# Optimization experiments

Measured on AMD Instinct MI355X. Metric: run time of the kernel, lower is better.

The kernel has to match this reference:

```python
import jax, jax.numpy as jnp
import numpy as np

E, DM, DH, K, DIL = 8, 512, 1024, 3, 2
N, L = 128, 128
PAD = DIL * (K - 1) // 2  # 'same' padding


def _conv1d(x, w):
    # x: [N, Cin, L], w: [Cout, Cin, K] -> [N, Cout, L]
    return jax.lax.conv_general_dilated(
        x, w, window_strides=(1,), padding=[(PAD, PAD)],
        rhs_dilation=(DIL,), dimension_numbers=("NCH", "OIH", "NCH"))


def _moe_conv(x, W, B, onehot):
    # W: [E, Cout, Cin, K], B: [E, Cout], onehot: [N, E]
    ys = jax.vmap(lambda w, b: _conv1d(x, w) + b[None, :, None])(W, B)  # [E, N, Cout, L]
    return jnp.einsum("enol,ne->nol", ys, onehot)


def setup_inputs() -> dict:
    key = jax.random.key(0)
    k1, k2, k3, k4, k5 = jax.random.split(key, 5)
    inp = jax.random.normal(k1, (N, DM, L), dtype=jnp.float32)
    # uneven per-expert sample counts summing to N (samples pre-sorted by expert)
    fwd_expert_count = jnp.asarray(np.array([10, 20, 16, 16, 12, 22, 14, 18], dtype=np.int32))
    w1 = jax.random.normal(k2, (E, DH, DM, K), dtype=jnp.float32) * 0.02
    b1 = jax.random.normal(k3, (E, DH), dtype=jnp.float32) * 0.02
    w2 = jax.random.normal(k4, (E, DM, DH, K), dtype=jnp.float32) * 0.02
    b2 = jax.random.normal(k5, (E, DM), dtype=jnp.float32) * 0.02
    return {"inp": inp, "fwd_expert_count": fwd_expert_count,
            "w1": w1, "b1": b1, "w2": w2, "b2": b2}


def reference(inp, fwd_expert_count, w1, b1, w2, b2):
    # map each sample index to its expert via cumulative counts
    cs = jnp.cumsum(fwd_expert_count)
    eid = jnp.searchsorted(cs, jnp.arange(N), side="right")  # [N]
    onehot = (eid[:, None] == jnp.arange(E)[None, :]).astype(inp.dtype)  # [N, E]
    h = _moe_conv(inp, w1, b1, onehot)       # [N, DH, L]
    h = jax.nn.gelu(h)
    out = _moe_conv(h, w2, b2, onehot)       # [N, DM, L]
    return out
```

## Files before the change

### kernel.cpp

```cpp
#include <hip/hip_runtime.h>
#include <hip/hip_bf16.h>
#include <stdint.h>


typedef __attribute__((ext_vector_type(8))) short short8;
typedef __attribute__((ext_vector_type(4))) float f32x4;

#define DMV 512
#define DHV 1024

#define OFF_X   0ull
#define OFF_H   (16ull << 20)
#define OFF_W1  (48ull << 20)
#define OFF_W2  (72ull << 20)

#define VMW(n) asm volatile("s_waitcnt vmcnt(" #n ")" ::: "memory")
#define VMNOP  do {} while (0)

__device__ __forceinline__ uint16_t f2bf(float f) {
  uint32_t u = __builtin_bit_cast(uint32_t, f);
  uint32_t r = (u + 0x7FFFu + ((u >> 16) & 1u)) >> 16;
  return (uint16_t)r;
}

__device__ __forceinline__ void async_copy16(const void* g, void* l) {
  __builtin_amdgcn_global_load_lds(
      (const __attribute__((address_space(1))) uint32_t*)g,
      (__attribute__((address_space(3))) uint32_t*)l, 16, 0, 0);
}

__device__ __forceinline__ float gelu_f(float x) {
  float u = 0.7978845608028654f * (x + 0.044715f * x * x * x);
  float t = __expf(2.0f * u);
  float th = 1.0f - 2.0f / (t + 1.0f);
  return 0.5f * x * (1.0f + th);
}

__global__ __launch_bounds__(256) void prep_x_t(const float* __restrict__ inp,
                                                uint16_t* __restrict__ xp) {
  uint32_t b = blockIdx.x;
  uint32_t s = b >> 4, cc = b & 15u;
  __shared__ uint16_t xs[32][132];
  uint32_t t = threadIdx.x;
  const float* src0 = inp + ((size_t)s * DMV + cc * 32u) * 128u;
#pragma unroll
  for (int i = 0; i < 4; ++i) {
    uint32_t idx = (uint32_t)i * 256u + t;
    uint32_t ch = idx >> 5, l4 = idx & 31u;
    float4 f = *(const float4*)(src0 + ch * 128u + l4 * 4u);
    uint2 pk;
    pk.x = (uint32_t)f2bf(f.x) | ((uint32_t)f2bf(f.y) << 16);
    pk.y = (uint32_t)f2bf(f.z) | ((uint32_t)f2bf(f.w) << 16);
    *(uint2*)&xs[ch][l4 * 4u] = pk;
  }
  __syncthreads();
  uint32_t l = t >> 1, half = t & 1u;
  uint32_t fl = ((l + 2u) >> 1) & 3u;
#pragma unroll
  for (int hi = 0; hi < 2; ++hi) {
    uint32_t sub = half * 2u + (uint32_t)hi;
    uint32_t cg = (sub ^ fl) & 3u;
    uint32_t pk[4];
#pragma unroll
    for (int p2 = 0; p2 < 4; ++p2) {
      uint32_t c0 = cg * 8u + (uint32_t)p2 * 2u;
      pk[p2] = (uint32_t)xs[c0][l] | ((uint32_t)xs[c0 + 1][l] << 16);
    }
    uint4 v; v.x = pk[0]; v.y = pk[1]; v.z = pk[2]; v.w = pk[3];
    size_t slot = (((size_t)s * 16u + cc) * 128u + l) * 4u + sub;
    *(uint4*)(xp + slot * 8u) = v;
  }
}

template <int LOGCG, int LOGO>
__global__ __launch_bounds__(256) void prep_w_c(const float* __restrict__ w,
                                                uint16_t* __restrict__ wp) {
  constexpr uint32_t C = 4u << LOGCG;
  constexpr uint32_t CCn = C >> 5;
  constexpr uint32_t MTn = 1u << (LOGO - 7);
  uint32_t t = blockIdx.x * 256u + threadIdx.x;
  uint32_t cg = t & ((1u << LOGCG) - 1u);
  uint32_t o = (t >> LOGCG) & ((1u << LOGO) - 1u);
  uint32_t e = t >> (LOGCG + LOGO);
  uint32_t row = o & 127u, mt = o >> 7;
  const float* src = w + (((size_t)(e << LOGO) + o) * C + cg * 4u) * 3u;
  float4 f0 = *(const float4*)(src);
  float4 f1 = *(const float4*)(src + 4);
  float4 f2 = *(const float4*)(src + 8);
  uint32_t cc = cg >> 3;
  uint32_t sub = ((cg >> 1) & 3u) ^ ((row >> 1) & 3u);
  uint32_t j0 = (cg & 1u) * 4u;
  size_t base = (((size_t)e * CCn + cc) * MTn + mt) * 3u;
  uint2 q;
  q.x = (uint32_t)f2bf(f0.x) | ((uint32_t)f2bf(f0.w) << 16);
  q.y = (uint32_t)f2bf(f1.z) | ((uint32_t)f2bf(f2.y) << 16);
  *(uint2*)(wp + ((base + 0u) * 128u + row) * 32u + sub * 8u + j0) = q;
  q.x = (uint32_t)f2bf(f0.y) | ((uint32_t)f2bf(f1.x) << 16);
  q.y = (uint32_t)f2bf(f1.w) | ((uint32_t)f2bf(f2.z) << 16);
  *(uint2*)(wp + ((base + 1u) * 128u + row) * 32u + sub * 8u + j0) = q;
  q.x = (uint32_t)f2bf(f0.z) | ((uint32_t)f2bf(f1.y) << 16);
  q.y = (uint32_t)f2bf(f2.x) | ((uint32_t)f2bf(f2.w) << 16);
  *(uint2*)(wp + ((base + 2u) * 128u + row) * 32u + sub * 8u + j0) = q;
}

#define PHASE_STEP(K, STAGE_BODY, VM_BODY)                                     \
  {                                                                            \
    short8 af_[4], bf_[4];                                                     \
    _Pragma("unroll") for (int q = 0; q < 4; ++q)                              \
      af_[q] = *(const short8*)(br + aOff[q] + (uint32_t)(K) * 8192u);         \
    _Pragma("unroll") for (int bq = 0; bq < 4; ++bq) {                         \
      uint32_t r_ = lB[bq] + 2u * (uint32_t)(K);                               \
      bf_[bq] = *(const short8*)(br + 24576u + r_ * 64u +                      \
                  (((uint32_t)kg ^ (r_ >> 1)) & 3u) * 16u);                    \
    }                                                                          \
    STAGE_BODY;                                                                \
    VM_BODY;                                                                   \
    __builtin_amdgcn_s_barrier();                                              \
    asm volatile("s_waitcnt lgkmcnt(0)" ::: "memory");                         \
    __builtin_amdgcn_s_setprio(1);                                             \
    _Pragma("unroll") for (int q = 0; q < 4; ++q)                              \
      _Pragma("unroll") for (int bq = 0; bq < 4; ++bq)                         \
        acc[q][bq] = __builtin_amdgcn_mfma_f32_16x16x32_bf16(                  \
            af_[q], bf_[bq], acc[q][bq], 0, 0, 0);                             \
    __builtin_amdgcn_s_setprio(0);                                             \
    __builtin_amdgcn_s_barrier();                                              \
  }

template <int PHASE>
__global__ __launch_bounds__(256, 2) void conv_mfma(
    const uint16_t* __restrict__ bprep, const uint16_t* __restrict__ wprep,
    const float* __restrict__ bias, const int* __restrict__ cnt,
    uint16_t* __restrict__ hout, float* __restrict__ fout) {
  constexpr int CC = (PHASE == 1) ? 16 : 32;
  constexpr int MTP = (PHASE == 1) ? 8 : 4;
  constexpr int OO = (PHASE == 1) ? DHV : DMV;
  constexpr uint32_t BUFS = 24576u + 8448u;

  uint32_t b = blockIdx.x;
  constexpr uint32_t CPX = (128u * MTP) >> 3;
  uint32_t work = (b & 7u) * CPX + (b >> 3);
  const int s = work & 127;
  const int mt = work >> 7;
  int e = 0;
  {
    int cum = cnt[0];
    while (s >= cum && e < 7) { ++e; cum += cnt[e]; }
  }
  const int tid = threadIdx.x;
  const int lane = tid & 63;
  const int wv = tid >> 6;
  const int wr = wv >> 1, wc = wv & 1;
  const int l15 = lane & 15, kg = lane >> 4;

  __shared__ __align__(16) uint8_t lds[2 * BUFS];

  uint32_t aOff[4];
#pragma unroll
  for (int a = 0; a < 4; ++a) {
    uint32_t ri = (uint32_t)(wr * 64 + a * 16 + l15);
    aOff[a] = ri * 64u + (((uint32_t)kg ^ (ri >> 1)) & 3u) * 16u;
  }
  uint32_t lB[4];
#pragma unroll
  for (int bq = 0; bq < 4; ++bq) lB[bq] = (uint32_t)(wc * 64 + bq * 16 + l15);

  const uint16_t* wTile0 = wprep + ((size_t)e * CC * MTP + mt) * 12288;
  auto SA = [&](uint8_t* bw, int ccn, int k, int h) {
    async_copy16(wTile0 + (size_t)ccn * (MTP * 12288) + k * 4096 + h * 2048 + tid * 8,
                 bw + (uint32_t)k * 8192u + (uint32_t)h * 4096u + (uint32_t)tid * 16);
  };
  auto SBL = [&](uint8_t* bw, int ccn, int h) {
    async_copy16(bprep + ((size_t)s * CC + ccn) * 4096 + h * 2048 + tid * 8,
                 bw + 24576u + 128u + (uint32_t)h * 4096u + (uint32_t)tid * 16);
  };

  if (tid < 32) {
    uint32_t n = (uint32_t)tid >> 4, ri = ((uint32_t)tid >> 2) & 3u, sb = (uint32_t)tid & 3u;
    uint32_t rowByte = (ri < 2) ? ri * 64u : (8320u + (ri - 2) * 64u);
    uint4 z = make_uint4(0, 0, 0, 0);
    *(uint4*)(lds + n * BUFS + 24576u + rowByte + sb * 16u) = z;
  }

  SBL(lds, 0, 0); SBL(lds, 0, 1);
  SA(lds, 0, 0, 0); SA(lds, 0, 0, 1);
  SA(lds, 0, 1, 0); SA(lds, 0, 1, 1);
  SA(lds, 0, 2, 0); SA(lds, 0, 2, 1);
  VMW(4);
  asm volatile("s_waitcnt lgkmcnt(0)" ::: "memory");
  __builtin_amdgcn_s_barrier();

  f32x4 acc[4][4] = {};

#pragma unroll 1
  for (int cc = 0; cc < CC - 1; ++cc) {
    const uint8_t* br = lds + (uint32_t)(cc & 1) * BUFS;
    uint8_t* bw = lds + (uint32_t)((cc & 1) ^ 1) * BUFS;
    const int cn = cc + 1;
    PHASE_STEP(0, { SBL(bw, cn, 0); SBL(bw, cn, 1); SA(bw, cn, 0, 0); SA(bw, cn, 0, 1); }, VMW(6));
    PHASE_STEP(1, { SA(bw, cn, 1, 0); SA(bw, cn, 1, 1); }, VMW(6));
    PHASE_STEP(2, { SA(bw, cn, 2, 0); SA(bw, cn, 2, 1); }, VMW(4));
  }
  {
    const uint8_t* br = lds + (uint32_t)((CC - 1) & 1) * BUFS;
    PHASE_STEP(0, {}, VMW(2));
    PHASE_STEP(1, {}, VMW(0));
    PHASE_STEP(2, {}, VMNOP);
  }

  if (PHASE == 1) {
#pragma unroll
    for (int a = 0; a < 4; ++a) {
      int ob = mt * 128 + wr * 64 + a * 16 + kg * 4;
      float4 bv = *(const float4*)(bias + (size_t)e * OO + ob);
      int cc2 = mt * 4 + wr * 2 + (a >> 1);
      uint32_t g = (uint32_t)((a & 1) * 2 + (kg >> 1));
      uint32_t j0 = (uint32_t)((kg & 1) * 4);
#pragma unroll
      for (int bq = 0; bq < 4; ++bq) {
        int l = wc * 64 + bq * 16 + l15;
        uint32_t flq = ((uint32_t)(l + 2) >> 1) & 3u;
        uint32_t sub = g ^ flq;
        float v0 = gelu_f(acc[a][bq][0] + bv.x);
        float v1 = gelu_f(acc[a][bq][1] + bv.y);
        float v2 = gelu_f(acc[a][bq][2] + bv.z);
        float v3 = gelu_f(acc[a][bq][3] + bv.w);
        uint2 pk;
        pk.x = (uint32_t)f2bf(v0) | ((uint32_t)f2bf(v1) << 16);
        pk.y = (uint32_t)f2bf(v2) | ((uint32_t)f2bf(v3) << 16);
        size_t ci = ((size_t)s * 32 + cc2) * 128 + l;
        *(uint2*)(hout + ci * 32 + sub * 8 + j0) = pk;
      }
    }
  } else {
#pragma unroll
    for (int a = 0; a < 4; ++a) {
      int ob = mt * 128 + wr * 64 + a * 16 + kg * 4;
      float4 bv = *(const float4*)(bias + (size_t)e * OO + ob);
      float bvr[4] = {bv.x, bv.y, bv.z, bv.w};
      float* op = fout + ((size_t)s * DMV + ob) * 128;
#pragma unroll
      for (int bq = 0; bq < 4; ++bq) {
        int l = wc * 64 + bq * 16 + l15;
#pragma unroll
        for (int r = 0; r < 4; ++r)
          op[(size_t)r * 128 + l] = acc[a][bq][r] + bvr[r];
      }
    }
  }
}

extern "C" void kernel_launch(void* const* d_in, const int* in_sizes, int n_in,
                              void* d_out, int out_size, void* d_ws, size_t ws_size,
                              hipStream_t stream) {
  const float* inp = (const float*)d_in[0];
  const int* cnt = (const int*)d_in[1];
  const float* w1 = (const float*)d_in[2];
  const float* b1 = (const float*)d_in[3];
  const float* w2 = (const float*)d_in[4];
  const float* b2 = (const float*)d_in[5];
  float* out = (float*)d_out;
  uint8_t* ws = (uint8_t*)d_ws;
  uint16_t* xp = (uint16_t*)(ws + OFF_X);
  uint16_t* hp = (uint16_t*)(ws + OFF_H);
  uint16_t* w1p = (uint16_t*)(ws + OFF_W1);
  uint16_t* w2p = (uint16_t*)(ws + OFF_W2);

  prep_x_t<<<dim3(2048), dim3(256), 0, stream>>>(inp, xp);
  prep_w_c<7, 10><<<dim3(4096), dim3(256), 0, stream>>>(w1, w1p);
  prep_w_c<8, 9><<<dim3(4096), dim3(256), 0, stream>>>(w2, w2p);
  conv_mfma<1><<<dim3(1024), dim3(256), 0, stream>>>(xp, w1p, b1, cnt, hp, nullptr);
  conv_mfma<2><<<dim3(512), dim3(256), 0, stream>>>(hp, w2p, b2, cnt, nullptr, out);
}
```

Before: 142.1 us.

## Simplify double-buffered conv pipeline to one barrier per channel chunk

Replaces the three-step-per-chunk pipeline with a simpler scheme. Each chunk issues the whole next-chunk prefetch up front, runs all three tap MFMA groups without intermediate barriers or priority toggles, then waits for all loads and synchronizes once. This cuts the barrier count from six per chunk to one and removes the fine-grained vmcnt staging. The cost is that load completion is no longer staggered against compute, so exposed memory latency may grow.

```diff
diff --git a/kernel.cpp b/kernel.cpp
--- a/kernel.cpp
+++ b/kernel.cpp
@@ -15,7 +15,6 @@
 #define OFF_W2  (72ull << 20)
 
 #define VMW(n) asm volatile("s_waitcnt vmcnt(" #n ")" ::: "memory")
-#define VMNOP  do {} while (0)
 
 __device__ __forceinline__ uint16_t f2bf(float f) {
   uint32_t u = __builtin_bit_cast(uint32_t, f);
@@ -103,29 +102,6 @@
   *(uint2*)(wp + ((base + 2u) * 128u + row) * 32u + sub * 8u + j0) = q;
 }
 
-#define PHASE_STEP(K, STAGE_BODY, VM_BODY)                                     \
-  {                                                                            \
-    short8 af_[4], bf_[4];                                                     \
-    _Pragma("unroll") for (int q = 0; q < 4; ++q)                              \
-      af_[q] = *(const short8*)(br + aOff[q] + (uint32_t)(K) * 8192u);         \
-    _Pragma("unroll") for (int bq = 0; bq < 4; ++bq) {                         \
-      uint32_t r_ = lB[bq] + 2u * (uint32_t)(K);                               \
-      bf_[bq] = *(const short8*)(br + 24576u + r_ * 64u +                      \
-                  (((uint32_t)kg ^ (r_ >> 1)) & 3u) * 16u);                    \
-    }                                                                          \
-    STAGE_BODY;                                                                \
-    VM_BODY;                                                                   \
-    __builtin_amdgcn_s_barrier();                                              \
-    asm volatile("s_waitcnt lgkmcnt(0)" ::: "memory");                         \
-    __builtin_amdgcn_s_setprio(1);                                             \
-    _Pragma("unroll") for (int q = 0; q < 4; ++q)                              \
-      _Pragma("unroll") for (int bq = 0; bq < 4; ++bq)                         \
-        acc[q][bq] = __builtin_amdgcn_mfma_f32_16x16x32_bf16(                  \
-            af_[q], bf_[bq], acc[q][bq], 0, 0, 0);                             \
-    __builtin_amdgcn_s_setprio(0);                                             \
-    __builtin_amdgcn_s_barrier();                                              \
-  }
-
 template <int PHASE>
 __global__ __launch_bounds__(256, 2) void conv_mfma(
     const uint16_t* __restrict__ bprep, const uint16_t* __restrict__ wprep,
@@ -173,6 +149,12 @@
     async_copy16(bprep + ((size_t)s * CC + ccn) * 4096 + h * 2048 + tid * 8,
                  bw + 24576u + 128u + (uint32_t)h * 4096u + (uint32_t)tid * 16);
   };
+  auto STAGE = [&](uint8_t* bw, int ccn) {
+    SBL(bw, ccn, 0); SBL(bw, ccn, 1);
+    SA(bw, ccn, 0, 0); SA(bw, ccn, 0, 1);
+    SA(bw, ccn, 1, 0); SA(bw, ccn, 1, 1);
+    SA(bw, ccn, 2, 0); SA(bw, ccn, 2, 1);
+  };
 
   if (tid < 32) {
     uint32_t n = (uint32_t)tid >> 4, ri = ((uint32_t)tid >> 2) & 3u, sb = (uint32_t)tid & 3u;
@@ -181,30 +163,43 @@
     *(uint4*)(lds + n * BUFS + 24576u + rowByte + sb * 16u) = z;
   }
 
-  SBL(lds, 0, 0); SBL(lds, 0, 1);
-  SA(lds, 0, 0, 0); SA(lds, 0, 0, 1);
-  SA(lds, 0, 1, 0); SA(lds, 0, 1, 1);
-  SA(lds, 0, 2, 0); SA(lds, 0, 2, 1);
-  VMW(4);
+  STAGE(lds, 0);
+  VMW(0);
   asm volatile("s_waitcnt lgkmcnt(0)" ::: "memory");
   __builtin_amdgcn_s_barrier();
+  asm volatile("" ::: "memory");
 
   f32x4 acc[4][4] = {};
 
 #pragma unroll 1
-  for (int cc = 0; cc < CC - 1; ++cc) {
+  for (int cc = 0; cc < CC; ++cc) {
     const uint8_t* br = lds + (uint32_t)(cc & 1) * BUFS;
     uint8_t* bw = lds + (uint32_t)((cc & 1) ^ 1) * BUFS;
-    const int cn = cc + 1;
-    PHASE_STEP(0, { SBL(bw, cn, 0); SBL(bw, cn, 1); SA(bw, cn, 0, 0); SA(bw, cn, 0, 1); }, VMW(6));
-    PHASE_STEP(1, { SA(bw, cn, 1, 0); SA(bw, cn, 1, 1); }, VMW(6));
-    PHASE_STEP(2, { SA(bw, cn, 2, 0); SA(bw, cn, 2, 1); }, VMW(4));
-  }
-  {
-    const uint8_t* br = lds + (uint32_t)((CC - 1) & 1) * BUFS;
-    PHASE_STEP(0, {}, VMW(2));
-    PHASE_STEP(1, {}, VMW(0));
-    PHASE_STEP(2, {}, VMNOP);
+    if (cc + 1 < CC) STAGE(bw, cc + 1);
+#pragma unroll
+    for (int k = 0; k < 3; ++k) {
+      short8 af_[4], bf_[4];
+#pragma unroll
+      for (int q = 0; q < 4; ++q)
+        af_[q] = *(const short8*)(br + aOff[q] + (uint32_t)k * 8192u);
+#pragma unroll
+      for (int bq = 0; bq < 4; ++bq) {
+        uint32_t r_ = lB[bq] + 2u * (uint32_t)k;
+        bf_[bq] = *(const short8*)(br + 24576u + r_ * 64u +
+                                   (((uint32_t)kg ^ (r_ >> 1)) & 3u) * 16u);
+      }
+#pragma unroll
+      for (int q = 0; q < 4; ++q)
+#pragma unroll
+        for (int bq = 0; bq < 4; ++bq)
+          acc[q][bq] = __builtin_amdgcn_mfma_f32_16x16x32_bf16(
+              af_[q], bf_[bq], acc[q][bq], 0, 0, 0);
+    }
+    if (cc + 1 < CC) {
+      VMW(0);
+      __builtin_amdgcn_s_barrier();
+      asm volatile("" ::: "memory");
+    }
   }
 
   if (PHASE == 1) {
```

After: 146.5 us. 3.1% more time.
